# Kernel optimization log

Measured on AMD Instinct MI355X. Metric: run time of the kernel, lower is better.

Reference implementation:

```python
import jax, jax.numpy as jnp
import numpy as np

EMBED_DIM = 2048
HEAD_DIM = 128            # __init__ head_dim arg
HALF = HEAD_DIM // 2      # internal self.head_dim = 64
NH2 = EMBED_DIM // HALF   # 32 q/k heads
H = NH2 // 2              # 16 differential heads
DEPTH = 12
LAMBDA_INIT = 0.8 - 0.6 * float(np.exp(-0.3 * DEPTH))
SCALING = HEAD_DIM ** (-0.5)   # source divides scores by this (== *sqrt(head_dim))
BATCH, SEQ = 1, 2048
EPS = 1e-5


def setup_inputs() -> dict:
    key = jax.random.key(0)
    ks = jax.random.split(key, 10)
    wstd = 0.25 / float(np.sqrt(EMBED_DIM))  # keep logits moderate despite *sqrt(head_dim)
    return {
        "x": jax.random.normal(ks[0], (BATCH, SEQ, EMBED_DIM), jnp.float32),
        "wq": jax.random.normal(ks[1], (EMBED_DIM, EMBED_DIM), jnp.float32) * wstd,
        "wk": jax.random.normal(ks[2], (EMBED_DIM, EMBED_DIM), jnp.float32) * wstd,
        "wv": jax.random.normal(ks[3], (EMBED_DIM, EMBED_DIM), jnp.float32) * wstd,
        "wout": jax.random.normal(ks[4], (EMBED_DIM, EMBED_DIM), jnp.float32) * wstd,
        "lambda_q1": jax.random.normal(ks[5], (HALF,), jnp.float32) * 0.1,
        "lambda_q2": jax.random.normal(ks[6], (HALF,), jnp.float32) * 0.1,
        "lambda_k1": jax.random.normal(ks[7], (HALF,), jnp.float32) * 0.1,
        "lambda_k2": jax.random.normal(ks[8], (HALF,), jnp.float32) * 0.1,
        "subln_weight": jnp.ones((2 * HALF,), jnp.float32),
    }


def _rope_tables(t, dim):
    # precompute_freqs_cis: freqs = 1/theta^(arange(0,dim,2)/dim); angles = outer(t, freqs)
    inv = 1.0 / (10000.0 ** (np.arange(0, dim, 2)[: dim // 2].astype(np.float64) / dim))
    ang = np.outer(np.arange(t), inv)
    return jnp.asarray(np.cos(ang), jnp.float32), jnp.asarray(np.sin(ang), jnp.float32)


def _apply_rope(x, cos, sin):
    # x: [b, t, h, d]; interleaved (even, odd) pairs form complex numbers
    xr, xi = x[..., 0::2], x[..., 1::2]
    c = cos[None, :, None, :]
    s = sin[None, :, None, :]
    out = jnp.stack([xr * c - xi * s, xr * s + xi * c], axis=-1)
    return out.reshape(x.shape)


def reference(x, wq, wk, wv, wout, lambda_q1, lambda_q2, lambda_k1, lambda_k2, subln_weight):
    b, t, e = x.shape
    # nn.Linear(bias=False): y = x @ W^T
    q = (x @ wq.T).reshape(b, t, NH2, HALF)
    k = (x @ wk.T).reshape(b, t, NH2, HALF)
    v = (x @ wv.T).reshape(b, t, H, 2 * HALF)  # intended DIFF-attn layout
    cos, sin = _rope_tables(t, HALF)
    q = _apply_rope(q, cos, sin)
    k = _apply_rope(k, cos, sin)
    q = q.transpose(0, 2, 1, 3)  # [b, 2H, t, HALF]
    k = k.transpose(0, 2, 1, 3)
    v = v.transpose(0, 2, 1, 3)  # [b, H, t, 2*HALF]
    # source: attn_weights = qk / scaling  (scaling = head_dim**-0.5 -> multiply by sqrt(head_dim))
    scores = jnp.einsum('bhtd,bhsd->bhts', q, k) / SCALING
    # default attn_mask = triu(zeros) == all zeros -> no masking applied
    probs = jax.nn.softmax(scores, axis=-1)
    lam1 = jnp.exp(jnp.sum(lambda_q1 * lambda_k1))
    lam2 = jnp.exp(jnp.sum(lambda_q2 * lambda_k2))
    lam = lam1 - lam2 + LAMBDA_INIT
    probs = probs.reshape(b, H, 2, t, t)
    diff = probs[:, :, 0] - lam * probs[:, :, 1]        # [b, H, t, t]
    attn = jnp.einsum('bhts,bhsd->bhtd', diff, v)        # [b, H, t, 2*HALF]
    # RMSNorm(2*HALF, eps=1e-5)
    attn = attn * jax.lax.rsqrt(jnp.mean(attn * attn, axis=-1, keepdims=True) + EPS)
    attn = attn * subln_weight
    attn = attn.transpose(0, 2, 1, 3).reshape(b, t, e)
    return attn @ wout.T
```

## Files before the change

kernel.cpp:

```cpp
#include <hip/hip_runtime.h>
#include <math.h>

#define SEQ 2048
#define EMB 2048

typedef _Float16 f16;
typedef unsigned short ushort_t;
typedef __attribute__((ext_vector_type(2))) _Float16 f16x2;
typedef __attribute__((ext_vector_type(4))) _Float16 f16x4;
typedef __attribute__((ext_vector_type(8))) _Float16 f16x8;
typedef __attribute__((ext_vector_type(4))) float f32x4;
typedef __attribute__((ext_vector_type(16))) float f32x16;
typedef __attribute__((ext_vector_type(8))) short bf16x8;
typedef __attribute__((ext_vector_type(4))) unsigned short us4;
typedef __attribute__((ext_vector_type(8))) unsigned short us8;
typedef __attribute__((ext_vector_type(4))) unsigned int uint4v;

__device__ __forceinline__ void gload16(const void* g, void* l) {
  __builtin_amdgcn_global_load_lds((const __attribute__((address_space(1))) unsigned int*)g,
                                   (__attribute__((address_space(3))) unsigned int*)l, 16, 0, 0);
}

__device__ __forceinline__ ushort_t f32_to_bf16(float f) {
  unsigned int u = __builtin_bit_cast(unsigned int, f);
  u += 0x7FFFu + ((u >> 16) & 1u);
  return (ushort_t)(u >> 16);
}

__device__ __forceinline__ unsigned cvt_pk_bf16_2(float lo, float hi) {
  unsigned r;
  asm("v_cvt_pk_bf16_f32 %0, %1, %2" : "=v"(r) : "v"(lo), "v"(hi));
  return r;
}

__global__ __launch_bounds__(256) void cvt5_kernel(const float* __restrict__ i0,
                                                   const float* __restrict__ i1,
                                                   const float* __restrict__ i2,
                                                   const float* __restrict__ i3,
                                                   const float* __restrict__ i4,
                                                   f16* __restrict__ o0, f16* __restrict__ o1,
                                                   f16* __restrict__ o2, f16* __restrict__ o3,
                                                   f16* __restrict__ o4) {
  int b = blockIdx.x;
  int z = b >> 12;
  const float* in = (z == 0) ? i0 : (z == 1) ? i1 : (z == 2) ? i2 : (z == 3) ? i3 : i4;
  f16* out = (z == 0) ? o0 : (z == 1) ? o1 : (z == 2) ? o2 : (z == 3) ? o3 : o4;
  int i = ((b & 4095) * 256 + threadIdx.x) * 4;
  f32x4 v = *(const f32x4*)(in + i);
  *(f16x4*)(out + i) = __builtin_convertvector(v, f16x4);
}

__global__ __launch_bounds__(256) void rope_table_kernel(float* __restrict__ cosT,
                                                         float* __restrict__ sinT) {
  int id = blockIdx.x * 256 + threadIdx.x;
  int t = id >> 5, i = id & 31;
  double inv = pow(10000.0, -(double)i / 32.0);
  double ang = (double)t * inv;
  cosT[id] = (float)cos(ang);
  sinT[id] = (float)sin(ang);
}

__global__ __launch_bounds__(256) void rope2_kernel(f16* __restrict__ q, f16* __restrict__ k,
                                                    const float* __restrict__ cosT,
                                                    const float* __restrict__ sinT) {
  f16* x = blockIdx.y ? k : q;
  const float scale = blockIdx.y ? 1.0f : 16.3222307f;
  int id = blockIdx.x * 256 + threadIdx.x;
  int i = id & 31;
  int nh2 = (id >> 5) & 31;
  int t = id >> 10;
  float c = cosT[(t << 5) + i], s = sinT[(t << 5) + i];
  int base = t * EMB + nh2 * 64 + 2 * i;
  f16x2 p = *(f16x2*)(x + base);
  float xr = (float)p.x, xi = (float)p.y;
  f16x2 o;
  o.x = (f16)((xr * c - xi * s) * scale);
  o.y = (f16)((xr * s + xi * c) * scale);
  *(f16x2*)(x + base) = o;
}

__global__ __launch_bounds__(256, 3) void proj_gemm_kernel(
    const f16* __restrict__ A, const f16* __restrict__ B0, const f16* __restrict__ B1,
    const f16* __restrict__ B2, f16* __restrict__ qout, f16* __restrict__ kout,
    ushort_t* __restrict__ vtout) {
  const int z = blockIdx.z;
  const f16* __restrict__ B = (z == 0) ? B0 : ((z == 1) ? B1 : B2);
  __shared__ f16 As[128 * 32];
  __shared__ f16 Bs[128 * 32];
  const int tid = threadIdx.x;
  const int wave = tid >> 6, lane = tid & 63;
  const int l16 = lane & 15, quad = lane >> 4;
  const int wm = (wave >> 1) << 6, wn = (wave & 1) << 6;
  const int bm = blockIdx.y << 7, bn = blockIdx.x << 7;

  const int swg = ((lane & 3) ^ ((lane >> 3) & 3)) * 8;
  const f16* Ag = A + (size_t)(bm + wave * 32 + (lane >> 2)) * EMB + swg;
  const f16* Bg = B + (size_t)(bn + wave * 32 + (lane >> 2)) * EMB + swg;
  f16* Asl = &As[wave * 1024 + lane * 8];
  f16* Bsl = &Bs[wave * 1024 + lane * 8];

  const int swr = (quad ^ ((l16 >> 1) & 3)) * 8;
  int aoff[4], boff[4];
#pragma unroll
  for (int i = 0; i < 4; i++) {
    aoff[i] = (wm + i * 16 + l16) * 32 + swr;
    boff[i] = (wn + i * 16 + l16) * 32 + swr;
  }

  f32x4 acc[4][4];
#pragma unroll
  for (int i = 0; i < 4; i++)
#pragma unroll
    for (int j = 0; j < 4; j++) acc[i][j] = (f32x4){0.f, 0.f, 0.f, 0.f};

  for (int k0 = 0; k0 < EMB; k0 += 32) {
    __syncthreads();
    gload16(Ag + k0, Asl);
    gload16(Ag + (size_t)16 * EMB + k0, Asl + 512);
    gload16(Bg + k0, Bsl);
    gload16(Bg + (size_t)16 * EMB + k0, Bsl + 512);
    __syncthreads();
    f16x8 af[4], bf[4];
#pragma unroll
    for (int mi = 0; mi < 4; mi++) af[mi] = *(const f16x8*)&As[aoff[mi]];
#pragma unroll
    for (int ni = 0; ni < 4; ni++) bf[ni] = *(const f16x8*)&Bs[boff[ni]];
#pragma unroll
    for (int mi = 0; mi < 4; mi++)
#pragma unroll
      for (int ni = 0; ni < 4; ni++)
        acc[mi][ni] = __builtin_amdgcn_mfma_f32_16x16x32_f16(af[mi], bf[ni], acc[mi][ni], 0, 0, 0);
  }

#pragma unroll
  for (int mi = 0; mi < 4; mi++) {
#pragma unroll
    for (int ni = 0; ni < 4; ni++) {
      int row0 = bm + wm + mi * 16 + quad * 4;
      int col = bn + wn + ni * 16 + l16;
      if (z == 2) {
        us4 o;
#pragma unroll
        for (int rg = 0; rg < 4; rg++) o[rg] = f32_to_bf16(acc[mi][ni][rg]);
        int hidx = col >> 7, d = col & 127, t = row0;
        size_t idx = ((((size_t)hidx * 32 + (t >> 6)) * 4 + ((t >> 4) & 3)) * 4 + (d >> 5)) * 512 +
                     (((t >> 3) & 1) * 32 + (d & 31)) * 8 + (t & 7);
        *(us4*)&vtout[idx] = o;
      } else {
        f16* Co = (z == 0) ? qout : kout;
#pragma unroll
        for (int rg = 0; rg < 4; rg++)
          Co[(size_t)(row0 + rg) * EMB + col] = (f16)acc[mi][ni][rg];
      }
    }
  }
}

__global__ __launch_bounds__(256, 2) void out_gemm_kernel(const f16* __restrict__ A,
                                                          const f16* __restrict__ B,
                                                          float* __restrict__ C) {
  __shared__ f16 As[128 * 32];
  __shared__ f16 Bs[64 * 32];
  const int tid = threadIdx.x;
  const int wave = tid >> 6, lane = tid & 63;
  const int l16 = lane & 15, quad = lane >> 4;
  const int wm = (wave >> 1) << 6, wn = (wave & 1) << 5;
  const int bm = blockIdx.y << 7, bn = blockIdx.x << 6;

  const int swg = ((lane & 3) ^ ((lane >> 3) & 3)) * 8;
  const f16* Ag = A + (size_t)(bm + wave * 32 + (lane >> 2)) * EMB + swg;
  const f16* Bg = B + (size_t)(bn + wave * 16 + (lane >> 2)) * EMB + swg;
  f16* Asl = &As[wave * 1024 + lane * 8];
  f16* Bsl = &Bs[wave * 512 + lane * 8];

  const int swr = (quad ^ ((l16 >> 1) & 3)) * 8;
  int aoff[4], boff[2];
#pragma unroll
  for (int i = 0; i < 4; i++) aoff[i] = (wm + i * 16 + l16) * 32 + swr;
#pragma unroll
  for (int i = 0; i < 2; i++) boff[i] = (wn + i * 16 + l16) * 32 + swr;

  f32x4 acc[4][2];
#pragma unroll
  for (int i = 0; i < 4; i++)
#pragma unroll
    for (int j = 0; j < 2; j++) acc[i][j] = (f32x4){0.f, 0.f, 0.f, 0.f};

  for (int k0 = 0; k0 < EMB; k0 += 32) {
    __syncthreads();
    gload16(Ag + k0, Asl);
    gload16(Ag + (size_t)16 * EMB + k0, Asl + 512);
    gload16(Bg + k0, Bsl);
    __syncthreads();
    f16x8 af[4], bf[2];
#pragma unroll
    for (int mi = 0; mi < 4; mi++) af[mi] = *(const f16x8*)&As[aoff[mi]];
#pragma unroll
    for (int ni = 0; ni < 2; ni++) bf[ni] = *(const f16x8*)&Bs[boff[ni]];
#pragma unroll
    for (int mi = 0; mi < 4; mi++)
#pragma unroll
      for (int ni = 0; ni < 2; ni++)
        acc[mi][ni] = __builtin_amdgcn_mfma_f32_16x16x32_f16(af[mi], bf[ni], acc[mi][ni], 0, 0, 0);
  }

#pragma unroll
  for (int mi = 0; mi < 4; mi++) {
#pragma unroll
    for (int ni = 0; ni < 2; ni++) {
      int row0 = bm + wm + mi * 16 + quad * 4;
      int col = bn + wn + ni * 16 + l16;
#pragma unroll
      for (int rg = 0; rg < 4; rg++)
        C[(size_t)(row0 + rg) * EMB + col] = acc[mi][ni][rg];
    }
  }
}

__global__ __launch_bounds__(256, 2) void diff_attn_v6(
    const f16* __restrict__ qb, const f16* __restrict__ kb, const ushort_t* __restrict__ vbT,
    const float* __restrict__ lq1, const float* __restrict__ lq2,
    const float* __restrict__ lk1, const float* __restrict__ lk2,
    const float* __restrict__ subw, f16* __restrict__ attnb) {
  const int h = blockIdx.x;
  const int qblk = blockIdx.y;
  const int tid = threadIdx.x;
  const int wave = tid >> 6, lane = tid & 63;
  const int l32 = lane & 31, hi = lane >> 5;
  const int hh = wave >> 1, qs = wave & 1;

  __shared__ f16 Ks[2][8192];
  __shared__ ushort_t Vt[2][8192];

  const int qrow0 = qblk * 64 + qs * 32;
  f16x8 qf[4];
#pragma unroll
  for (int c = 0; c < 4; c++)
    qf[c] = *(const f16x8*)(qb + (size_t)(qrow0 + l32) * EMB + h * 128 + hh * 64 + c * 16 + hi * 8);

  f32x16 O[4];
#pragma unroll
  for (int dt = 0; dt < 4; dt++)
#pragma unroll
    for (int s2 = 0; s2 < 16; s2++) O[dt][s2] = 0.f;
  float lsum = 0.f;

  const int hhs = wave >> 1, kbs = wave & 1;
  const f16* kgp = kb + (size_t)(kbs * 32 + l32) * EMB + h * 128 + hhs * 64 + hi * 8;
  const ushort_t* vgp = vbT + ((size_t)h * 32) * 8192 + (size_t)wave * 2048 + lane * 8;

#pragma unroll
  for (int j2 = 0; j2 < 4; j2++) gload16(kgp + j2 * 16, &Ks[0][(wave * 4 + j2) * 512]);
#pragma unroll
  for (int j2 = 0; j2 < 4; j2++) gload16(vgp + j2 * 512, &Vt[0][(wave * 4 + j2) * 512]);
  __syncthreads();

  auto step = [&](int cbuf, int nit) {
    if (nit < 32) {
#pragma unroll
      for (int j2 = 0; j2 < 4; j2++)
        gload16(kgp + (size_t)nit * (64 * EMB) + j2 * 16, &Ks[cbuf ^ 1][(wave * 4 + j2) * 512]);
#pragma unroll
      for (int j2 = 0; j2 < 4; j2++)
        gload16(vgp + (size_t)nit * 8192 + j2 * 512, &Vt[cbuf ^ 1][(wave * 4 + j2) * 512]);
    }

    const f16* KsC = &Ks[cbuf][0];
    const ushort_t* VtC = &Vt[cbuf][0];
    bf16x8 pf[4];

#pragma unroll
    for (int kbi = 0; kbi < 2; kbi++) {
      f32x16 acc;
#pragma unroll
      for (int s2 = 0; s2 < 16; s2++) acc[s2] = -28.8539008f;
#pragma unroll
      for (int c = 0; c < 4; c++) {
        f16x8 kf = *(const f16x8*)&KsC[(hh * 8 + kbi * 4 + c) * 512 + lane * 8];
        acc = __builtin_amdgcn_mfma_f32_32x32x16_f16(kf, qf[c], acc, 0, 0, 0);
      }
      float p[16];
#pragma unroll
      for (int s2 = 0; s2 < 16; s2++) p[s2] = __builtin_exp2f(acc[s2]);
      lsum += (((p[0] + p[1]) + (p[2] + p[3])) + ((p[4] + p[5]) + (p[6] + p[7]))) +
              (((p[8] + p[9]) + (p[10] + p[11])) + ((p[12] + p[13]) + (p[14] + p[15])));
#pragma unroll
      for (int c2 = 0; c2 < 2; c2++) {
        unsigned w0 = cvt_pk_bf16_2(p[8 * c2 + 0], p[8 * c2 + 1]);
        unsigned w1 = cvt_pk_bf16_2(p[8 * c2 + 2], p[8 * c2 + 3]);
        unsigned w2 = cvt_pk_bf16_2(p[8 * c2 + 4], p[8 * c2 + 5]);
        unsigned w3 = cvt_pk_bf16_2(p[8 * c2 + 6], p[8 * c2 + 7]);
        asm("v_permlane32_swap_b32 %0, %1" : "+v"(w0), "+v"(w2));
        asm("v_permlane32_swap_b32 %0, %1" : "+v"(w1), "+v"(w3));
        uint4v pw;
        pw.x = w0; pw.y = w1; pw.z = w2; pw.w = w3;
        pf[kbi * 2 + c2] = __builtin_bit_cast(bf16x8, pw);
      }
    }

#pragma unroll
    for (int kc = 0; kc < 4; kc++) {
#pragma unroll
      for (int dt = 0; dt < 4; dt++) {
        bf16x8 vf = *(const bf16x8*)&VtC[(kc * 4 + dt) * 512 + lane * 8];
        O[dt] = __builtin_amdgcn_mfma_f32_32x32x16_bf16(vf, pf[kc], O[dt], 0, 0, 0);
      }
    }
    __syncthreads();
  };

  for (int it = 0; it < 32; it += 2) {
    step(0, it + 1);
    step(1, it + 2);
  }

  float d1 = 0.f, d2 = 0.f;
  for (int i = 0; i < 64; i++) {
    d1 += lq1[i] * lk1[i];
    d2 += lq2[i] * lk2[i];
  }
  const float lam = __expf(d1) - __expf(d2) + 0.783605767f;

  float s = lsum + __shfl_xor(lsum, 32);
  const float inv = (hh == 0) ? (1.f / s) : (lam / s);

  float* Obuf = (float*)&Ks[0][0];
  if (hh == 1) {
#pragma unroll
    for (int dt = 0; dt < 4; dt++)
#pragma unroll
      for (int rq = 0; rq < 4; rq++) {
        f32x4 v;
#pragma unroll
        for (int rg = 0; rg < 4; rg++) v[rg] = O[dt][rq * 4 + rg] * inv;
        *(f32x4*)&Obuf[(((qs * 4 + dt) * 4 + rq) * 64 + lane) * 4] = v;
      }
  }
  __syncthreads();
  if (hh == 0) {
    float a[4][16];
    float ms = 0.f;
#pragma unroll
    for (int dt = 0; dt < 4; dt++)
#pragma unroll
      for (int rq = 0; rq < 4; rq++) {
        f32x4 o1 = *(const f32x4*)&Obuf[(((qs * 4 + dt) * 4 + rq) * 64 + lane) * 4];
#pragma unroll
        for (int rg = 0; rg < 4; rg++) {
          float v = O[dt][rq * 4 + rg] * inv - o1[rg];
          a[dt][rq * 4 + rg] = v;
          ms += v * v;
        }
      }
    ms += __shfl_xor(ms, 32);
    const float rms = rsqrtf(ms * (1.f / 128.f) + 1e-5f);
    const int t_g = qrow0 + l32;
#pragma unroll
    for (int dt = 0; dt < 4; dt++)
#pragma unroll
      for (int rq = 0; rq < 4; rq++) {
        f32x4 sw = *(const f32x4*)(subw + dt * 32 + rq * 8 + hi * 4);
        f16x4 o;
#pragma unroll
        for (int rg = 0; rg < 4; rg++) o[rg] = (f16)(a[dt][rq * 4 + rg] * rms * sw[rg]);
        *(f16x4*)(attnb + (size_t)t_g * EMB + h * 128 + dt * 32 + rq * 8 + hi * 4) = o;
      }
  }
}

extern "C" void kernel_launch(void* const* d_in, const int* in_sizes, int n_in,
                              void* d_out, int out_size, void* d_ws, size_t ws_size,
                              hipStream_t stream) {
  const float* x    = (const float*)d_in[0];
  const float* wq   = (const float*)d_in[1];
  const float* wk   = (const float*)d_in[2];
  const float* wv   = (const float*)d_in[3];
  const float* wout = (const float*)d_in[4];
  const float* lq1  = (const float*)d_in[5];
  const float* lq2  = (const float*)d_in[6];
  const float* lk1  = (const float*)d_in[7];
  const float* lk2  = (const float*)d_in[8];
  const float* subw = (const float*)d_in[9];
  float* out = (float*)d_out;

  char* ws = (char*)d_ws;
  const size_t MB = 1024 * 1024;
  f16* xb    = (f16*)(ws + 0 * MB);
  f16* wqb   = (f16*)(ws + 8 * MB);
  f16* wkb   = (f16*)(ws + 16 * MB);
  f16* wvb   = (f16*)(ws + 24 * MB);
  f16* woutb = (f16*)(ws + 32 * MB);
  f16* qb    = (f16*)(ws + 40 * MB);
  f16* kb    = (f16*)(ws + 48 * MB);
  ushort_t* vbT = (ushort_t*)(ws + 56 * MB);
  f16* attnb = (f16*)(ws + 64 * MB);
  float* cosT = (float*)(ws + 72 * MB);
  float* sinT = (float*)(ws + 72 * MB + 262144);

  dim3 b256(256);
  cvt5_kernel<<<5 * 4096, b256, 0, stream>>>(x, wq, wk, wv, wout, xb, wqb, wkb, wvb, woutb);
  rope_table_kernel<<<256, b256, 0, stream>>>(cosT, sinT);

  proj_gemm_kernel<<<dim3(16, 16, 3), b256, 0, stream>>>(xb, wqb, wkb, wvb, qb, kb, vbT);

  rope2_kernel<<<dim3(8192, 2), b256, 0, stream>>>(qb, kb, cosT, sinT);

  diff_attn_v6<<<dim3(16, 32), b256, 0, stream>>>(qb, kb, vbT, lq1, lq2, lk1, lk2, subw, attnb);

  out_gemm_kernel<<<dim3(32, 16), b256, 0, stream>>>(attnb, woutb, out);
}
```

Before: 309.6 us.

## Split attention KV tile across 8 waves with cross-wave reduction

The attention block grows from 4 to 8 waves. Each wave pair now handles half of the 64-key tile (split-K within the tile), and partial O and row sums are reduced through shared memory at the end. K and V staging is divided between wave groups, and the PV MFMAs are wrapped in s_setprio. The aim is more waves per CU to hide exp/convert latency and more MFMA parallelism, at the cost of extra epilogue reduction, barriers, and LDS traffic.

```diff
diff --git a/kernel.cpp b/kernel.cpp
--- a/kernel.cpp
+++ b/kernel.cpp
@@ -217,7 +217,7 @@
   }
 }
 
-__global__ __launch_bounds__(256, 2) void diff_attn_v6(
+__global__ __launch_bounds__(512, 4) void diff_attn_v7(
     const f16* __restrict__ qb, const f16* __restrict__ kb, const ushort_t* __restrict__ vbT,
     const float* __restrict__ lq1, const float* __restrict__ lq2,
     const float* __restrict__ lk1, const float* __restrict__ lk2,
@@ -227,10 +227,12 @@
   const int tid = threadIdx.x;
   const int wave = tid >> 6, lane = tid & 63;
   const int l32 = lane & 31, hi = lane >> 5;
-  const int hh = wave >> 1, qs = wave & 1;
-
-  __shared__ f16 Ks[2][8192];
-  __shared__ ushort_t Vt[2][8192];
+  const int ks = wave >> 2, hh = (wave >> 1) & 1, qs = wave & 1;
+
+  __shared__ __align__(16) char smem[65536];
+  __shared__ float lsb[128];
+  f16* Ks0 = (f16*)smem;
+  ushort_t* Vt0 = (ushort_t*)(smem + 32768);
 
   const int qrow0 = qblk * 64 + qs * 32;
   f16x8 qf[4];
@@ -245,67 +247,71 @@
     for (int s2 = 0; s2 < 16; s2++) O[dt][s2] = 0.f;
   float lsum = 0.f;
 
-  const int hhs = wave >> 1, kbs = wave & 1;
-  const f16* kgp = kb + (size_t)(kbs * 32 + l32) * EMB + h * 128 + hhs * 64 + hi * 8;
-  const ushort_t* vgp = vbT + ((size_t)h * 32) * 8192 + (size_t)wave * 2048 + lane * 8;
-
-#pragma unroll
-  for (int j2 = 0; j2 < 4; j2++) gload16(kgp + j2 * 16, &Ks[0][(wave * 4 + j2) * 512]);
-#pragma unroll
-  for (int j2 = 0; j2 < 4; j2++) gload16(vgp + j2 * 512, &Vt[0][(wave * 4 + j2) * 512]);
+  const bool isK = (wave < 4);
+  const f16* kgp =
+      kb + (size_t)((wave & 1) * 32 + l32) * EMB + h * 128 + ((wave >> 1) & 1) * 64 + hi * 8;
+  const ushort_t* vgp = vbT + (size_t)h * 262144 + (size_t)(wave & 3) * 2048 + lane * 8;
+
+  auto stage = [&](int buf, int it) {
+    if (isK) {
+      const f16* src = kgp + (size_t)it * (64 * EMB);
+      f16* dst = Ks0 + buf * 8192 + wave * 2048;
+#pragma unroll
+      for (int j2 = 0; j2 < 4; j2++) gload16(src + j2 * 16, dst + j2 * 512);
+    } else {
+      const ushort_t* src = vgp + (size_t)it * 8192;
+      ushort_t* dst = Vt0 + buf * 8192 + (wave - 4) * 2048;
+#pragma unroll
+      for (int j2 = 0; j2 < 4; j2++) gload16(src + j2 * 512, dst + j2 * 512);
+    }
+  };
+
+  stage(0, 0);
   __syncthreads();
 
   auto step = [&](int cbuf, int nit) {
-    if (nit < 32) {
-#pragma unroll
-      for (int j2 = 0; j2 < 4; j2++)
-        gload16(kgp + (size_t)nit * (64 * EMB) + j2 * 16, &Ks[cbuf ^ 1][(wave * 4 + j2) * 512]);
-#pragma unroll
-      for (int j2 = 0; j2 < 4; j2++)
-        gload16(vgp + (size_t)nit * 8192 + j2 * 512, &Vt[cbuf ^ 1][(wave * 4 + j2) * 512]);
-    }
-
-    const f16* KsC = &Ks[cbuf][0];
-    const ushort_t* VtC = &Vt[cbuf][0];
-    bf16x8 pf[4];
-
-#pragma unroll
-    for (int kbi = 0; kbi < 2; kbi++) {
-      f32x16 acc;
-#pragma unroll
-      for (int s2 = 0; s2 < 16; s2++) acc[s2] = -28.8539008f;
-#pragma unroll
-      for (int c = 0; c < 4; c++) {
-        f16x8 kf = *(const f16x8*)&KsC[(hh * 8 + kbi * 4 + c) * 512 + lane * 8];
-        acc = __builtin_amdgcn_mfma_f32_32x32x16_f16(kf, qf[c], acc, 0, 0, 0);
-      }
-      float p[16];
-#pragma unroll
-      for (int s2 = 0; s2 < 16; s2++) p[s2] = __builtin_exp2f(acc[s2]);
-      lsum += (((p[0] + p[1]) + (p[2] + p[3])) + ((p[4] + p[5]) + (p[6] + p[7]))) +
-              (((p[8] + p[9]) + (p[10] + p[11])) + ((p[12] + p[13]) + (p[14] + p[15])));
-#pragma unroll
-      for (int c2 = 0; c2 < 2; c2++) {
-        unsigned w0 = cvt_pk_bf16_2(p[8 * c2 + 0], p[8 * c2 + 1]);
-        unsigned w1 = cvt_pk_bf16_2(p[8 * c2 + 2], p[8 * c2 + 3]);
-        unsigned w2 = cvt_pk_bf16_2(p[8 * c2 + 4], p[8 * c2 + 5]);
-        unsigned w3 = cvt_pk_bf16_2(p[8 * c2 + 6], p[8 * c2 + 7]);
-        asm("v_permlane32_swap_b32 %0, %1" : "+v"(w0), "+v"(w2));
-        asm("v_permlane32_swap_b32 %0, %1" : "+v"(w1), "+v"(w3));
-        uint4v pw;
-        pw.x = w0; pw.y = w1; pw.z = w2; pw.w = w3;
-        pf[kbi * 2 + c2] = __builtin_bit_cast(bf16x8, pw);
-      }
-    }
-
-#pragma unroll
-    for (int kc = 0; kc < 4; kc++) {
+    if (nit < 32) stage(cbuf ^ 1, nit);
+
+    const f16* KsC = Ks0 + cbuf * 8192;
+    const ushort_t* VtC = Vt0 + cbuf * 8192;
+
+    f32x16 acc;
+#pragma unroll
+    for (int s2 = 0; s2 < 16; s2++) acc[s2] = -28.8539008f;
+#pragma unroll
+    for (int c = 0; c < 4; c++) {
+      f16x8 kf = *(const f16x8*)&KsC[(hh * 8 + ks * 4 + c) * 512 + lane * 8];
+      acc = __builtin_amdgcn_mfma_f32_32x32x16_f16(kf, qf[c], acc, 0, 0, 0);
+    }
+    float p[16];
+#pragma unroll
+    for (int s2 = 0; s2 < 16; s2++) p[s2] = __builtin_exp2f(acc[s2]);
+    lsum += (((p[0] + p[1]) + (p[2] + p[3])) + ((p[4] + p[5]) + (p[6] + p[7]))) +
+            (((p[8] + p[9]) + (p[10] + p[11])) + ((p[12] + p[13]) + (p[14] + p[15])));
+    bf16x8 pf[2];
+#pragma unroll
+    for (int c2 = 0; c2 < 2; c2++) {
+      unsigned w0 = cvt_pk_bf16_2(p[8 * c2 + 0], p[8 * c2 + 1]);
+      unsigned w1 = cvt_pk_bf16_2(p[8 * c2 + 2], p[8 * c2 + 3]);
+      unsigned w2 = cvt_pk_bf16_2(p[8 * c2 + 4], p[8 * c2 + 5]);
+      unsigned w3 = cvt_pk_bf16_2(p[8 * c2 + 6], p[8 * c2 + 7]);
+      asm("v_permlane32_swap_b32 %0, %1" : "+v"(w0), "+v"(w2));
+      asm("v_permlane32_swap_b32 %0, %1" : "+v"(w1), "+v"(w3));
+      uint4v pw;
+      pw.x = w0; pw.y = w1; pw.z = w2; pw.w = w3;
+      pf[c2] = __builtin_bit_cast(bf16x8, pw);
+    }
+
+    __builtin_amdgcn_s_setprio(1);
+#pragma unroll
+    for (int c2 = 0; c2 < 2; c2++) {
 #pragma unroll
       for (int dt = 0; dt < 4; dt++) {
-        bf16x8 vf = *(const bf16x8*)&VtC[(kc * 4 + dt) * 512 + lane * 8];
-        O[dt] = __builtin_amdgcn_mfma_f32_32x32x16_bf16(vf, pf[kc], O[dt], 0, 0, 0);
-      }
-    }
+        bf16x8 vf = *(const bf16x8*)&VtC[((ks * 2 + c2) * 4 + dt) * 512 + lane * 8];
+        O[dt] = __builtin_amdgcn_mfma_f32_32x32x16_bf16(vf, pf[c2], O[dt], 0, 0, 0);
+      }
+    }
+    __builtin_amdgcn_s_setprio(0);
     __syncthreads();
   };
 
@@ -321,33 +327,65 @@
   }
   const float lam = __expf(d1) - __expf(d2) + 0.783605767f;
 
-  float s = lsum + __shfl_xor(lsum, 32);
-  const float inv = (hh == 0) ? (1.f / s) : (lam / s);
-
-  float* Obuf = (float*)&Ks[0][0];
-  if (hh == 1) {
+  const float s_part = lsum + __shfl_xor(lsum, 32);
+
+  float* Obuf = (float*)smem;
+
+  if (ks == 1) {
+    float* ob = Obuf + (hh * 2 + qs) * 4096;
 #pragma unroll
     for (int dt = 0; dt < 4; dt++)
 #pragma unroll
       for (int rq = 0; rq < 4; rq++) {
         f32x4 v;
 #pragma unroll
-        for (int rg = 0; rg < 4; rg++) v[rg] = O[dt][rq * 4 + rg] * inv;
-        *(f32x4*)&Obuf[(((qs * 4 + dt) * 4 + rq) * 64 + lane) * 4] = v;
-      }
+        for (int rg = 0; rg < 4; rg++) v[rg] = O[dt][rq * 4 + rg];
+        *(f32x4*)&ob[(dt * 4 + rq) * 256 + lane * 4] = v;
+      }
+    lsb[(hh * 2 + qs) * 32 + l32] = s_part;
   }
   __syncthreads();
-  if (hh == 0) {
+
+  float inv_ = 0.f;
+  if (ks == 0) {
+    const float* ob = Obuf + (hh * 2 + qs) * 4096;
+#pragma unroll
+    for (int dt = 0; dt < 4; dt++)
+#pragma unroll
+      for (int rq = 0; rq < 4; rq++) {
+        f32x4 v1 = *(const f32x4*)&ob[(dt * 4 + rq) * 256 + lane * 4];
+#pragma unroll
+        for (int rg = 0; rg < 4; rg++) O[dt][rq * 4 + rg] += v1[rg];
+      }
+    const float s = s_part + lsb[(hh * 2 + qs) * 32 + l32];
+    inv_ = (hh == 0) ? (1.f / s) : (lam / s);
+  }
+  __syncthreads();
+
+  if (ks == 0 && hh == 1) {
+#pragma unroll
+    for (int dt = 0; dt < 4; dt++)
+#pragma unroll
+      for (int rq = 0; rq < 4; rq++) {
+        f32x4 v;
+#pragma unroll
+        for (int rg = 0; rg < 4; rg++) v[rg] = O[dt][rq * 4 + rg] * inv_;
+        *(f32x4*)&Obuf[((qs * 4 + dt) * 4 + rq) * 256 + lane * 4] = v;
+      }
+  }
+  __syncthreads();
+
+  if (ks == 0 && hh == 0) {
     float a[4][16];
     float ms = 0.f;
 #pragma unroll
     for (int dt = 0; dt < 4; dt++)
 #pragma unroll
       for (int rq = 0; rq < 4; rq++) {
-        f32x4 o1 = *(const f32x4*)&Obuf[(((qs * 4 + dt) * 4 + rq) * 64 + lane) * 4];
+        f32x4 o1 = *(const f32x4*)&Obuf[((qs * 4 + dt) * 4 + rq) * 256 + lane * 4];
 #pragma unroll
         for (int rg = 0; rg < 4; rg++) {
-          float v = O[dt][rq * 4 + rg] * inv - o1[rg];
+          float v = O[dt][rq * 4 + rg] * inv_ - o1[rg];
           a[dt][rq * 4 + rg] = v;
           ms += v * v;
         }
@@ -405,7 +443,8 @@
 
   rope2_kernel<<<dim3(8192, 2), b256, 0, stream>>>(qb, kb, cosT, sinT);
 
-  diff_attn_v6<<<dim3(16, 32), b256, 0, stream>>>(qb, kb, vbT, lq1, lq2, lk1, lk2, subw, attnb);
+  diff_attn_v7<<<dim3(16, 32), dim3(512), 0, stream>>>(qb, kb, vbT, lq1, lq2, lk1, lk2, subw,
+                                                       attnb);
 
   out_gemm_kernel<<<dim3(32, 16), b256, 0, stream>>>(attnb, woutb, out);
 }
```

After: 377.1 us. 21.8% more time.

## Split waves by key half instead of sub-head, sharing V fragments across both heads

Applied to the files above, without the earlier changes.

Each wave now handles both differential sub-heads for its query rows over half of each key block, rather than one sub-head over all keys. This lets each V fragment read from LDS feed two MFMAs (one per sub-head), cutting LDS V traffic per MFMA. The cost is a cross-wave reduction of softmax denominators through shared memory plus more registers (two Q fragment sets, two O accumulators). Priority raising via s_setprio around the PV MFMA block is also added.

```diff
diff --git a/kernel.cpp b/kernel.cpp
--- a/kernel.cpp
+++ b/kernel.cpp
@@ -217,7 +217,7 @@
   }
 }
 
-__global__ __launch_bounds__(256, 2) void diff_attn_v6(
+__global__ __launch_bounds__(256, 2) void diff_attn_v8(
     const f16* __restrict__ qb, const f16* __restrict__ kb, const ushort_t* __restrict__ vbT,
     const float* __restrict__ lq1, const float* __restrict__ lq2,
     const float* __restrict__ lk1, const float* __restrict__ lk2,
@@ -227,63 +227,79 @@
   const int tid = threadIdx.x;
   const int wave = tid >> 6, lane = tid & 63;
   const int l32 = lane & 31, hi = lane >> 5;
-  const int hh = wave >> 1, qs = wave & 1;
+  const int qs = wave >> 1, ks = wave & 1;
 
   __shared__ f16 Ks[2][8192];
   __shared__ ushort_t Vt[2][8192];
 
   const int qrow0 = qblk * 64 + qs * 32;
-  f16x8 qf[4];
-#pragma unroll
-  for (int c = 0; c < 4; c++)
-    qf[c] = *(const f16x8*)(qb + (size_t)(qrow0 + l32) * EMB + h * 128 + hh * 64 + c * 16 + hi * 8);
-
-  f32x16 O[4];
+  f16x8 qf[2][4];
+#pragma unroll
+  for (int hh = 0; hh < 2; hh++)
+#pragma unroll
+    for (int c = 0; c < 4; c++)
+      qf[hh][c] = *(const f16x8*)(qb + (size_t)(qrow0 + l32) * EMB + h * 128 + hh * 64 +
+                                  c * 16 + hi * 8);
+
+  f32x16 O0[4], O1[4];
 #pragma unroll
   for (int dt = 0; dt < 4; dt++)
 #pragma unroll
-    for (int s2 = 0; s2 < 16; s2++) O[dt][s2] = 0.f;
-  float lsum = 0.f;
-
-  const int hhs = wave >> 1, kbs = wave & 1;
-  const f16* kgp = kb + (size_t)(kbs * 32 + l32) * EMB + h * 128 + hhs * 64 + hi * 8;
-  const ushort_t* vgp = vbT + ((size_t)h * 32) * 8192 + (size_t)wave * 2048 + lane * 8;
-
-#pragma unroll
-  for (int j2 = 0; j2 < 4; j2++) gload16(kgp + j2 * 16, &Ks[0][(wave * 4 + j2) * 512]);
-#pragma unroll
-  for (int j2 = 0; j2 < 4; j2++) gload16(vgp + j2 * 512, &Vt[0][(wave * 4 + j2) * 512]);
+    for (int s2 = 0; s2 < 16; s2++) {
+      O0[dt][s2] = 0.f;
+      O1[dt][s2] = 0.f;
+    }
+  float lsum0 = 0.f, lsum1 = 0.f;
+
+  const f16* kgp =
+      kb + (size_t)((wave >> 1) * 32 + l32) * EMB + h * 128 + (wave & 1) * 64 + hi * 8;
+  const ushort_t* vgp = vbT + (size_t)h * 262144 + (size_t)wave * 2048 + lane * 8;
+
+  auto stage = [&](int buf, int it) {
+#pragma unroll
+    for (int j2 = 0; j2 < 4; j2++)
+      gload16(kgp + (size_t)it * (64 * EMB) + j2 * 16, &Ks[buf][(wave * 4 + j2) * 512]);
+#pragma unroll
+    for (int j2 = 0; j2 < 4; j2++)
+      gload16(vgp + (size_t)it * 8192 + j2 * 512, &Vt[buf][(wave * 4 + j2) * 512]);
+  };
+
+  stage(0, 0);
   __syncthreads();
 
   auto step = [&](int cbuf, int nit) {
-    if (nit < 32) {
-#pragma unroll
-      for (int j2 = 0; j2 < 4; j2++)
-        gload16(kgp + (size_t)nit * (64 * EMB) + j2 * 16, &Ks[cbuf ^ 1][(wave * 4 + j2) * 512]);
-#pragma unroll
-      for (int j2 = 0; j2 < 4; j2++)
-        gload16(vgp + (size_t)nit * 8192 + j2 * 512, &Vt[cbuf ^ 1][(wave * 4 + j2) * 512]);
-    }
+    if (nit < 32) stage(cbuf ^ 1, nit);
 
     const f16* KsC = &Ks[cbuf][0];
     const ushort_t* VtC = &Vt[cbuf][0];
-    bf16x8 pf[4];
-
-#pragma unroll
-    for (int kbi = 0; kbi < 2; kbi++) {
-      f32x16 acc;
-#pragma unroll
-      for (int s2 = 0; s2 < 16; s2++) acc[s2] = -28.8539008f;
-#pragma unroll
-      for (int c = 0; c < 4; c++) {
-        f16x8 kf = *(const f16x8*)&KsC[(hh * 8 + kbi * 4 + c) * 512 + lane * 8];
-        acc = __builtin_amdgcn_mfma_f32_32x32x16_f16(kf, qf[c], acc, 0, 0, 0);
-      }
+
+    f32x16 acc0, acc1;
+#pragma unroll
+    for (int s2 = 0; s2 < 16; s2++) {
+      acc0[s2] = -28.8539008f;
+      acc1[s2] = -28.8539008f;
+    }
+#pragma unroll
+    for (int c = 0; c < 4; c++) {
+      f16x8 kf = *(const f16x8*)&KsC[(ks * 8 + c) * 512 + lane * 8];
+      acc0 = __builtin_amdgcn_mfma_f32_32x32x16_f16(kf, qf[0][c], acc0, 0, 0, 0);
+    }
+#pragma unroll
+    for (int c = 0; c < 4; c++) {
+      f16x8 kf = *(const f16x8*)&KsC[(ks * 8 + 4 + c) * 512 + lane * 8];
+      acc1 = __builtin_amdgcn_mfma_f32_32x32x16_f16(kf, qf[1][c], acc1, 0, 0, 0);
+    }
+
+    bf16x8 pf[2][2];
+#pragma unroll
+    for (int hh = 0; hh < 2; hh++) {
       float p[16];
 #pragma unroll
-      for (int s2 = 0; s2 < 16; s2++) p[s2] = __builtin_exp2f(acc[s2]);
-      lsum += (((p[0] + p[1]) + (p[2] + p[3])) + ((p[4] + p[5]) + (p[6] + p[7]))) +
-              (((p[8] + p[9]) + (p[10] + p[11])) + ((p[12] + p[13]) + (p[14] + p[15])));
+      for (int s2 = 0; s2 < 16; s2++)
+        p[s2] = __builtin_exp2f(hh ? acc1[s2] : acc0[s2]);
+      float ls = (((p[0] + p[1]) + (p[2] + p[3])) + ((p[4] + p[5]) + (p[6] + p[7]))) +
+                 (((p[8] + p[9]) + (p[10] + p[11])) + ((p[12] + p[13]) + (p[14] + p[15])));
+      if (hh == 0) lsum0 += ls; else lsum1 += ls;
 #pragma unroll
       for (int c2 = 0; c2 < 2; c2++) {
         unsigned w0 = cvt_pk_bf16_2(p[8 * c2 + 0], p[8 * c2 + 1]);
@@ -294,18 +310,21 @@
         asm("v_permlane32_swap_b32 %0, %1" : "+v"(w1), "+v"(w3));
         uint4v pw;
         pw.x = w0; pw.y = w1; pw.z = w2; pw.w = w3;
-        pf[kbi * 2 + c2] = __builtin_bit_cast(bf16x8, pw);
-      }
-    }
-
-#pragma unroll
-    for (int kc = 0; kc < 4; kc++) {
+        pf[hh][c2] = __builtin_bit_cast(bf16x8, pw);
+      }
+    }
+
+    __builtin_amdgcn_s_setprio(1);
+#pragma unroll
+    for (int c2 = 0; c2 < 2; c2++) {
 #pragma unroll
       for (int dt = 0; dt < 4; dt++) {
-        bf16x8 vf = *(const bf16x8*)&VtC[(kc * 4 + dt) * 512 + lane * 8];
-        O[dt] = __builtin_amdgcn_mfma_f32_32x32x16_bf16(vf, pf[kc], O[dt], 0, 0, 0);
-      }
-    }
+        bf16x8 vf = *(const bf16x8*)&VtC[((ks * 2 + c2) * 4 + dt) * 512 + lane * 8];
+        O0[dt] = __builtin_amdgcn_mfma_f32_32x32x16_bf16(vf, pf[0][c2], O0[dt], 0, 0, 0);
+        O1[dt] = __builtin_amdgcn_mfma_f32_32x32x16_bf16(vf, pf[1][c2], O1[dt], 0, 0, 0);
+      }
+    }
+    __builtin_amdgcn_s_setprio(0);
     __syncthreads();
   };
 
@@ -321,34 +340,50 @@
   }
   const float lam = __expf(d1) - __expf(d2) + 0.783605767f;
 
-  float s = lsum + __shfl_xor(lsum, 32);
-  const float inv = (hh == 0) ? (1.f / s) : (lam / s);
+  __shared__ float lsb[2][2][2][32];
+  {
+    float s0 = lsum0 + __shfl_xor(lsum0, 32);
+    float s1 = lsum1 + __shfl_xor(lsum1, 32);
+    if (hi == 0) {
+      lsb[0][qs][ks][l32] = s0;
+      lsb[1][qs][ks][l32] = s1;
+    }
+  }
+  __syncthreads();
+  const float den0 = lsb[0][qs][0][l32] + lsb[0][qs][1][l32];
+  const float den1 = lsb[1][qs][0][l32] + lsb[1][qs][1][l32];
+  const float inv0 = 1.f / den0;
+  const float inv1 = lam / den1;
 
   float* Obuf = (float*)&Ks[0][0];
-  if (hh == 1) {
+#pragma unroll
+  for (int dt = 0; dt < 4; dt++)
+#pragma unroll
+    for (int s2 = 0; s2 < 16; s2++) O0[dt][s2] = O0[dt][s2] * inv0 - O1[dt][s2] * inv1;
+
+  if (ks == 1) {
 #pragma unroll
     for (int dt = 0; dt < 4; dt++)
 #pragma unroll
       for (int rq = 0; rq < 4; rq++) {
         f32x4 v;
 #pragma unroll
-        for (int rg = 0; rg < 4; rg++) v[rg] = O[dt][rq * 4 + rg] * inv;
-        *(f32x4*)&Obuf[(((qs * 4 + dt) * 4 + rq) * 64 + lane) * 4] = v;
+        for (int rg = 0; rg < 4; rg++) v[rg] = O0[dt][rq * 4 + rg];
+        *(f32x4*)&Obuf[(qs * 8192) + (dt * 4 + rq) * 256 + lane * 4] = v;
       }
   }
   __syncthreads();
-  if (hh == 0) {
-    float a[4][16];
+  if (ks == 0) {
     float ms = 0.f;
 #pragma unroll
     for (int dt = 0; dt < 4; dt++)
 #pragma unroll
       for (int rq = 0; rq < 4; rq++) {
-        f32x4 o1 = *(const f32x4*)&Obuf[(((qs * 4 + dt) * 4 + rq) * 64 + lane) * 4];
+        f32x4 v1 = *(const f32x4*)&Obuf[(qs * 8192) + (dt * 4 + rq) * 256 + lane * 4];
 #pragma unroll
         for (int rg = 0; rg < 4; rg++) {
-          float v = O[dt][rq * 4 + rg] * inv - o1[rg];
-          a[dt][rq * 4 + rg] = v;
+          float v = O0[dt][rq * 4 + rg] + v1[rg];
+          O0[dt][rq * 4 + rg] = v;
           ms += v * v;
         }
       }
@@ -362,7 +397,7 @@
         f32x4 sw = *(const f32x4*)(subw + dt * 32 + rq * 8 + hi * 4);
         f16x4 o;
 #pragma unroll
-        for (int rg = 0; rg < 4; rg++) o[rg] = (f16)(a[dt][rq * 4 + rg] * rms * sw[rg]);
+        for (int rg = 0; rg < 4; rg++) o[rg] = (f16)(O0[dt][rq * 4 + rg] * rms * sw[rg]);
         *(f16x4*)(attnb + (size_t)t_g * EMB + h * 128 + dt * 32 + rq * 8 + hi * 4) = o;
       }
   }
@@ -405,7 +440,7 @@
 
   rope2_kernel<<<dim3(8192, 2), b256, 0, stream>>>(qb, kb, cosT, sinT);
 
-  diff_attn_v6<<<dim3(16, 32), b256, 0, stream>>>(qb, kb, vbT, lq1, lq2, lk1, lk2, subw, attnb);
+  diff_attn_v8<<<dim3(16, 32), b256, 0, stream>>>(qb, kb, vbT, lq1, lq2, lk1, lk2, subw, attnb);
 
   out_gemm_kernel<<<dim3(32, 16), b256, 0, stream>>>(attnb, woutb, out);
 }
```

After: 304.1 us. About the same (-1.8%).

## Fuse RoPE into projection GEMM epilogue and interleave softmax with PV MFMAs

Applied to the files above, without the earlier changes.

Applies the rotary embedding and q scaling directly in the q/k projection GEMM epilogue, using a lane xor-shuffle to pair even/odd elements, and removes the standalone rope kernel. This eliminates one kernel launch and a full read-modify-write pass over q and k. The attention inner step is also split so the exp/pack of one key half overlaps with the PV MFMAs of the other, with raised wave priority around the MFMA bursts. The epilogue gains per-element cos/sin table loads and shuffles.

```diff
diff --git a/kernel.cpp b/kernel.cpp
--- a/kernel.cpp
+++ b/kernel.cpp
@@ -60,29 +60,10 @@
   sinT[id] = (float)sin(ang);
 }
 
-__global__ __launch_bounds__(256) void rope2_kernel(f16* __restrict__ q, f16* __restrict__ k,
-                                                    const float* __restrict__ cosT,
-                                                    const float* __restrict__ sinT) {
-  f16* x = blockIdx.y ? k : q;
-  const float scale = blockIdx.y ? 1.0f : 16.3222307f;
-  int id = blockIdx.x * 256 + threadIdx.x;
-  int i = id & 31;
-  int nh2 = (id >> 5) & 31;
-  int t = id >> 10;
-  float c = cosT[(t << 5) + i], s = sinT[(t << 5) + i];
-  int base = t * EMB + nh2 * 64 + 2 * i;
-  f16x2 p = *(f16x2*)(x + base);
-  float xr = (float)p.x, xi = (float)p.y;
-  f16x2 o;
-  o.x = (f16)((xr * c - xi * s) * scale);
-  o.y = (f16)((xr * s + xi * c) * scale);
-  *(f16x2*)(x + base) = o;
-}
-
 __global__ __launch_bounds__(256, 3) void proj_gemm_kernel(
     const f16* __restrict__ A, const f16* __restrict__ B0, const f16* __restrict__ B1,
-    const f16* __restrict__ B2, f16* __restrict__ qout, f16* __restrict__ kout,
-    ushort_t* __restrict__ vtout) {
+    const f16* __restrict__ B2, const float* __restrict__ cosT, const float* __restrict__ sinT,
+    f16* __restrict__ qout, f16* __restrict__ kout, ushort_t* __restrict__ vtout) {
   const int z = blockIdx.z;
   const f16* __restrict__ B = (z == 0) ? B0 : ((z == 1) ? B1 : B2);
   __shared__ f16 As[128 * 32];
@@ -132,13 +113,13 @@
         acc[mi][ni] = __builtin_amdgcn_mfma_f32_16x16x32_f16(af[mi], bf[ni], acc[mi][ni], 0, 0, 0);
   }
 
-#pragma unroll
-  for (int mi = 0; mi < 4; mi++) {
-#pragma unroll
-    for (int ni = 0; ni < 4; ni++) {
-      int row0 = bm + wm + mi * 16 + quad * 4;
-      int col = bn + wn + ni * 16 + l16;
-      if (z == 2) {
+  if (z == 2) {
+#pragma unroll
+    for (int mi = 0; mi < 4; mi++) {
+#pragma unroll
+      for (int ni = 0; ni < 4; ni++) {
+        int row0 = bm + wm + mi * 16 + quad * 4;
+        int col = bn + wn + ni * 16 + l16;
         us4 o;
 #pragma unroll
         for (int rg = 0; rg < 4; rg++) o[rg] = f32_to_bf16(acc[mi][ni][rg]);
@@ -146,11 +127,31 @@
         size_t idx = ((((size_t)hidx * 32 + (t >> 6)) * 4 + ((t >> 4) & 3)) * 4 + (d >> 5)) * 512 +
                      (((t >> 3) & 1) * 32 + (d & 31)) * 8 + (t & 7);
         *(us4*)&vtout[idx] = o;
-      } else {
-        f16* Co = (z == 0) ? qout : kout;
-#pragma unroll
-        for (int rg = 0; rg < 4; rg++)
-          Co[(size_t)(row0 + rg) * EMB + col] = (f16)acc[mi][ni][rg];
+      }
+    }
+  } else {
+    f16* Co = (z == 0) ? qout : kout;
+    const float scale = (z == 0) ? 16.3222307f : 1.0f;
+#pragma unroll
+    for (int mi = 0; mi < 4; mi++) {
+#pragma unroll
+      for (int ni = 0; ni < 4; ni++) {
+        int row0 = bm + wm + mi * 16 + quad * 4;
+        int col = bn + wn + ni * 16 + l16;
+        int i_r = (col & 63) >> 1;
+        int odd = col & 1;
+#pragma unroll
+        for (int rg = 0; rg < 4; rg++) {
+          int t = row0 + rg;
+          float c = cosT[(t << 5) + i_r] * scale;
+          float s = sinT[(t << 5) + i_r] * scale;
+          float own = acc[mi][ni][rg];
+          float other = __shfl_xor(own, 1);
+          float xr = odd ? other : own;
+          float xi = odd ? own : other;
+          float outv = odd ? (xr * s + xi * c) : (xr * c - xi * s);
+          Co[(size_t)t * EMB + col] = (f16)outv;
+        }
       }
     }
   }
@@ -217,7 +218,7 @@
   }
 }
 
-__global__ __launch_bounds__(256, 2) void diff_attn_v6(
+__global__ __launch_bounds__(256, 2) void diff_attn_v9(
     const f16* __restrict__ qb, const f16* __restrict__ kb, const ushort_t* __restrict__ vbT,
     const float* __restrict__ lq1, const float* __restrict__ lq2,
     const float* __restrict__ lk1, const float* __restrict__ lk2,
@@ -249,63 +250,78 @@
   const f16* kgp = kb + (size_t)(kbs * 32 + l32) * EMB + h * 128 + hhs * 64 + hi * 8;
   const ushort_t* vgp = vbT + ((size_t)h * 32) * 8192 + (size_t)wave * 2048 + lane * 8;
 
-#pragma unroll
-  for (int j2 = 0; j2 < 4; j2++) gload16(kgp + j2 * 16, &Ks[0][(wave * 4 + j2) * 512]);
-#pragma unroll
-  for (int j2 = 0; j2 < 4; j2++) gload16(vgp + j2 * 512, &Vt[0][(wave * 4 + j2) * 512]);
+  auto stage = [&](int buf, int it) {
+#pragma unroll
+    for (int j2 = 0; j2 < 4; j2++)
+      gload16(kgp + (size_t)it * (64 * EMB) + j2 * 16, &Ks[buf][(wave * 4 + j2) * 512]);
+#pragma unroll
+    for (int j2 = 0; j2 < 4; j2++)
+      gload16(vgp + (size_t)it * 8192 + j2 * 512, &Vt[buf][(wave * 4 + j2) * 512]);
+  };
+
+  stage(0, 0);
   __syncthreads();
 
+  auto qk4 = [&](const f16* KsC, int kbi) {
+    f32x16 acc;
+#pragma unroll
+    for (int s2 = 0; s2 < 16; s2++) acc[s2] = -28.8539008f;
+#pragma unroll
+    for (int c = 0; c < 4; c++) {
+      f16x8 kf = *(const f16x8*)&KsC[(hh * 8 + kbi * 4 + c) * 512 + lane * 8];
+      acc = __builtin_amdgcn_mfma_f32_32x32x16_f16(kf, qf[c], acc, 0, 0, 0);
+    }
+    return acc;
+  };
+
+  auto exppack = [&](const f32x16& acc, bf16x8* pf2) {
+    float p[16];
+#pragma unroll
+    for (int s2 = 0; s2 < 16; s2++) p[s2] = __builtin_exp2f(acc[s2]);
+    lsum += (((p[0] + p[1]) + (p[2] + p[3])) + ((p[4] + p[5]) + (p[6] + p[7]))) +
+            (((p[8] + p[9]) + (p[10] + p[11])) + ((p[12] + p[13]) + (p[14] + p[15])));
+#pragma unroll
+    for (int c2 = 0; c2 < 2; c2++) {
+      unsigned w0 = cvt_pk_bf16_2(p[8 * c2 + 0], p[8 * c2 + 1]);
+      unsigned w1 = cvt_pk_bf16_2(p[8 * c2 + 2], p[8 * c2 + 3]);
+      unsigned w2 = cvt_pk_bf16_2(p[8 * c2 + 4], p[8 * c2 + 5]);
+      unsigned w3 = cvt_pk_bf16_2(p[8 * c2 + 6], p[8 * c2 + 7]);
+      asm("v_permlane32_swap_b32 %0, %1" : "+v"(w0), "+v"(w2));
+      asm("v_permlane32_swap_b32 %0, %1" : "+v"(w1), "+v"(w3));
+      uint4v pw;
+      pw.x = w0; pw.y = w1; pw.z = w2; pw.w = w3;
+      pf2[c2] = __builtin_bit_cast(bf16x8, pw);
+    }
+  };
+
+  auto pv2 = [&](const ushort_t* VtC, int kc0, const bf16x8* pf2) {
+#pragma unroll
+    for (int c2 = 0; c2 < 2; c2++) {
+#pragma unroll
+      for (int dt = 0; dt < 4; dt++) {
+        bf16x8 vf = *(const bf16x8*)&VtC[((kc0 + c2) * 4 + dt) * 512 + lane * 8];
+        O[dt] = __builtin_amdgcn_mfma_f32_32x32x16_bf16(vf, pf2[c2], O[dt], 0, 0, 0);
+      }
+    }
+  };
+
   auto step = [&](int cbuf, int nit) {
-    if (nit < 32) {
-#pragma unroll
-      for (int j2 = 0; j2 < 4; j2++)
-        gload16(kgp + (size_t)nit * (64 * EMB) + j2 * 16, &Ks[cbuf ^ 1][(wave * 4 + j2) * 512]);
-#pragma unroll
-      for (int j2 = 0; j2 < 4; j2++)
-        gload16(vgp + (size_t)nit * 8192 + j2 * 512, &Vt[cbuf ^ 1][(wave * 4 + j2) * 512]);
-    }
+    if (nit < 32) stage(cbuf ^ 1, nit);
 
     const f16* KsC = &Ks[cbuf][0];
     const ushort_t* VtC = &Vt[cbuf][0];
-    bf16x8 pf[4];
-
-#pragma unroll
-    for (int kbi = 0; kbi < 2; kbi++) {
-      f32x16 acc;
-#pragma unroll
-      for (int s2 = 0; s2 < 16; s2++) acc[s2] = -28.8539008f;
-#pragma unroll
-      for (int c = 0; c < 4; c++) {
-        f16x8 kf = *(const f16x8*)&KsC[(hh * 8 + kbi * 4 + c) * 512 + lane * 8];
-        acc = __builtin_amdgcn_mfma_f32_32x32x16_f16(kf, qf[c], acc, 0, 0, 0);
-      }
-      float p[16];
-#pragma unroll
-      for (int s2 = 0; s2 < 16; s2++) p[s2] = __builtin_exp2f(acc[s2]);
-      lsum += (((p[0] + p[1]) + (p[2] + p[3])) + ((p[4] + p[5]) + (p[6] + p[7]))) +
-              (((p[8] + p[9]) + (p[10] + p[11])) + ((p[12] + p[13]) + (p[14] + p[15])));
-#pragma unroll
-      for (int c2 = 0; c2 < 2; c2++) {
-        unsigned w0 = cvt_pk_bf16_2(p[8 * c2 + 0], p[8 * c2 + 1]);
-        unsigned w1 = cvt_pk_bf16_2(p[8 * c2 + 2], p[8 * c2 + 3]);
-        unsigned w2 = cvt_pk_bf16_2(p[8 * c2 + 4], p[8 * c2 + 5]);
-        unsigned w3 = cvt_pk_bf16_2(p[8 * c2 + 6], p[8 * c2 + 7]);
-        asm("v_permlane32_swap_b32 %0, %1" : "+v"(w0), "+v"(w2));
-        asm("v_permlane32_swap_b32 %0, %1" : "+v"(w1), "+v"(w3));
-        uint4v pw;
-        pw.x = w0; pw.y = w1; pw.z = w2; pw.w = w3;
-        pf[kbi * 2 + c2] = __builtin_bit_cast(bf16x8, pw);
-      }
-    }
-
-#pragma unroll
-    for (int kc = 0; kc < 4; kc++) {
-#pragma unroll
-      for (int dt = 0; dt < 4; dt++) {
-        bf16x8 vf = *(const bf16x8*)&VtC[(kc * 4 + dt) * 512 + lane * 8];
-        O[dt] = __builtin_amdgcn_mfma_f32_32x32x16_bf16(vf, pf[kc], O[dt], 0, 0, 0);
-      }
-    }
+
+    f32x16 acc0 = qk4(KsC, 0);
+    f32x16 acc1 = qk4(KsC, 1);
+    bf16x8 pfa[2], pfb[2];
+    exppack(acc0, pfa);
+    __builtin_amdgcn_s_setprio(1);
+    pv2(VtC, 0, pfa);
+    __builtin_amdgcn_s_setprio(0);
+    exppack(acc1, pfb);
+    __builtin_amdgcn_s_setprio(1);
+    pv2(VtC, 2, pfb);
+    __builtin_amdgcn_s_setprio(0);
     __syncthreads();
   };
 
@@ -401,11 +417,10 @@
   cvt5_kernel<<<5 * 4096, b256, 0, stream>>>(x, wq, wk, wv, wout, xb, wqb, wkb, wvb, woutb);
   rope_table_kernel<<<256, b256, 0, stream>>>(cosT, sinT);
 
-  proj_gemm_kernel<<<dim3(16, 16, 3), b256, 0, stream>>>(xb, wqb, wkb, wvb, qb, kb, vbT);
-
-  rope2_kernel<<<dim3(8192, 2), b256, 0, stream>>>(qb, kb, cosT, sinT);
-
-  diff_attn_v6<<<dim3(16, 32), b256, 0, stream>>>(qb, kb, vbT, lq1, lq2, lk1, lk2, subw, attnb);
+  proj_gemm_kernel<<<dim3(16, 16, 3), b256, 0, stream>>>(xb, wqb, wkb, wvb, cosT, sinT, qb, kb,
+                                                         vbT);
+
+  diff_attn_v9<<<dim3(16, 32), b256, 0, stream>>>(qb, kb, vbT, lq1, lq2, lk1, lk2, subw, attnb);
 
   out_gemm_kernel<<<dim3(32, 16), b256, 0, stream>>>(attnb, woutb, out);
 }
```

Measured after the change: 296.8 us. 4.1% less time.
